# Kernel tuning notes

Hardware: AMD Instinct MI355X
Metric: run time of the kernel (lower is better)

Reference implementation:

```python
import jax, jax.numpy as jnp
import numpy as np

H = 768
NH = 12
HD = H // NH
FF = 3072
E = 4
EPS = 1e-12


def _make_expert_params(key):
    ks = jax.random.split(key, 8)
    s = 0.02
    return {
        'wq': jax.random.normal(ks[0], (H, H), jnp.float32) * s,
        'wk': jax.random.normal(ks[1], (H, H), jnp.float32) * s,
        'wv': jax.random.normal(ks[2], (H, H), jnp.float32) * s,
        'wo': jax.random.normal(ks[3], (H, H), jnp.float32) * s,
        'bq': jnp.zeros((H,), jnp.float32),
        'bk': jnp.zeros((H,), jnp.float32),
        'bv': jnp.zeros((H,), jnp.float32),
        'bo': jnp.zeros((H,), jnp.float32),
        'ln1_g': jnp.ones((H,), jnp.float32),
        'ln1_b': jnp.zeros((H,), jnp.float32),
        'w1': jax.random.normal(ks[4], (H, FF), jnp.float32) * s,
        'b1': jnp.zeros((FF,), jnp.float32),
        'w2': jax.random.normal(ks[5], (FF, H), jnp.float32) * s,
        'b2': jnp.zeros((H,), jnp.float32),
        'ln2_g': jnp.ones((H,), jnp.float32),
        'ln2_b': jnp.zeros((H,), jnp.float32),
    }


def setup_inputs() -> dict:
    key = jax.random.key(0)
    k1, k2, kp = jax.random.split(key, 3)
    hidden_states = jax.random.normal(k1, (64, 128, H), jnp.float32)
    attention_mask = jnp.zeros((64, 128), jnp.float32)  # additive mask, 0 = attend
    centers = jax.random.normal(k2, (E, H), jnp.float32)
    pkeys = jax.random.split(kp, E)
    ps = [_make_expert_params(k) for k in pkeys]
    # stack expert params along leading axis for vectorized gather-by-expert
    params = {k: jnp.stack([p[k] for p in ps], axis=0) for k in ps[0]}
    out = {'hidden_states': hidden_states, 'attention_mask': attention_mask, 'centers': centers}
    out.update(params)
    return out


def _layernorm(x, g, b):
    mu = x.mean(-1, keepdims=True)
    var = ((x - mu) ** 2).mean(-1, keepdims=True)
    return (x - mu) * jax.lax.rsqrt(var + EPS) * g + b


def _encoder(x, mask, p):
    # x: [B,S,H], mask: [B,S] additive; p: per-sample expert params (leading dim B)
    B, S, _ = x.shape
    q = jnp.einsum('bsh,bhd->bsd', x, p['wq']) + p['bq'][:, None, :]
    k = jnp.einsum('bsh,bhd->bsd', x, p['wk']) + p['bk'][:, None, :]
    v = jnp.einsum('bsh,bhd->bsd', x, p['wv']) + p['bv'][:, None, :]
    q = q.reshape(B, S, NH, HD)
    k = k.reshape(B, S, NH, HD)
    v = v.reshape(B, S, NH, HD)
    scores = jnp.einsum('bqnd,bknd->bnqk', q, k) / np.sqrt(HD).astype(np.float32)
    scores = scores + mask[:, None, None, :]
    attn = jax.nn.softmax(scores, axis=-1)
    ctx = jnp.einsum('bnqk,bknd->bqnd', attn, v).reshape(B, S, H)
    att_out = jnp.einsum('bsh,bhd->bsd', ctx, p['wo']) + p['bo'][:, None, :]
    att_out = _layernorm(att_out + x, p['ln1_g'][:, None, :], p['ln1_b'][:, None, :])
    ffn = jnp.einsum('bsh,bhf->bsf', att_out, p['w1']) + p['b1'][:, None, :]
    ffn = jax.nn.gelu(ffn)
    ffn = jnp.einsum('bsf,bfh->bsh', ffn, p['w2']) + p['b2'][:, None, :]
    out = _layernorm(att_out + ffn, p['ln2_g'][:, None, :], p['ln2_b'][:, None, :])
    return out


def reference(hidden_states, attention_mask, centers,
              wq, wk, wv, wo, bq, bk, bv, bo, ln1_g, ln1_b,
              w1, b1, w2, b2, ln2_g, ln2_b):
    # routing: mean over seq, cdist to centers, argmin -> per-sentence expert id
    h_pca = hidden_states.mean(axis=1)  # [B,H]
    d2 = (jnp.sum(h_pca ** 2, -1, keepdims=True)
          - 2.0 * h_pca @ centers.T
          + jnp.sum(centers ** 2, -1)[None, :])
    eid = jnp.argmin(d2, axis=1)  # [B]
    params = {'wq': wq, 'wk': wk, 'wv': wv, 'wo': wo, 'bq': bq, 'bk': bk,
              'bv': bv, 'bo': bo, 'ln1_g': ln1_g, 'ln1_b': ln1_b,
              'w1': w1, 'b1': b1, 'w2': w2, 'b2': b2,
              'ln2_g': ln2_g, 'ln2_b': ln2_b}
    # gather per-sample expert params (jit-friendly, honors hard routing)
    psel = {k: v[eid] for k, v in params.items()}
    return _encoder(hidden_states, attention_mask, psel)
```

## Files before the change

kernel.cpp:

```cpp
#include <hip/hip_runtime.h>
#include <hip/hip_bf16.h>
#include <math.h>

#define HDIM 768
#define NHEAD 12
#define HEADD 64
#define FFDIM 3072
#define NEXP 4
#define SEQ 128
#define NB 64
#define QKVN 2304

typedef __attribute__((ext_vector_type(8))) _Float16 f16x8;
typedef __attribute__((ext_vector_type(4))) _Float16 f16x4;
typedef __attribute__((ext_vector_type(4))) float f32x4;

__device__ __forceinline__ float gelu_fast(float x) {
  float t = -1.5957691216057308f * x * __builtin_fmaf(0.044715f * x, x, 1.0f);
  return x * __builtin_amdgcn_rcpf(1.0f + __expf(t));
}

__device__ __forceinline__ void gld_lds16(const void* g, void* l) {
  __builtin_amdgcn_global_load_lds(
      (const __attribute__((address_space(1))) unsigned int*)g,
      (__attribute__((address_space(3))) unsigned int*)l, 16, 0, 0);
}

__global__ __launch_bounds__(256) void route_cvt_kernel(
    const float* __restrict__ hs, const float* __restrict__ centers,
    int* __restrict__ eid, _Float16* __restrict__ x16) {
  int b = blockIdx.x, t = threadIdx.x;
  __shared__ float hp[HDIM];
  __shared__ float dist[NEXP];
  const float* xb = hs + (size_t)b * SEQ * HDIM;
  _Float16* ob = x16 + (size_t)b * SEQ * HDIM;

  if (t < 192) {
    float p0 = 0.f, p1 = 0.f, p2 = 0.f, p3 = 0.f;
    for (int sq = 0; sq < SEQ; ++sq) {
      float4 v = ((const float4*)(xb + (size_t)sq * HDIM))[t];
      p0 += v.x; p1 += v.y; p2 += v.z; p3 += v.w;
      f16x4 h = {(_Float16)v.x, (_Float16)v.y, (_Float16)v.z, (_Float16)v.w};
      *(f16x4*)(ob + (size_t)sq * HDIM + t * 4) = h;
    }
    hp[t * 4 + 0] = p0 * (1.0f / SEQ);
    hp[t * 4 + 1] = p1 * (1.0f / SEQ);
    hp[t * 4 + 2] = p2 * (1.0f / SEQ);
    hp[t * 4 + 3] = p3 * (1.0f / SEQ);
  }
  if (t < NEXP) dist[t] = 0.f;
  __syncthreads();

  float pe[NEXP] = {0.f, 0.f, 0.f, 0.f};
  for (int h = t; h < HDIM; h += 256) {
    float v = hp[h];
#pragma unroll
    for (int e = 0; e < NEXP; ++e) {
      float d = v - centers[e * HDIM + h];
      pe[e] += d * d;
    }
  }
#pragma unroll
  for (int e = 0; e < NEXP; ++e) atomicAdd(&dist[e], pe[e]);
  __syncthreads();
  if (t == 0) {
    int best = 0; float bv = dist[0];
    for (int e = 1; e < NEXP; ++e) if (dist[e] < bv) { bv = dist[e]; best = e; }
    eid[b] = best;
  }
}

__device__ __forceinline__ void tr_tile(const float* __restrict__ ip,
                                        _Float16* __restrict__ op,
                                        int K, int N, int nb, int kb,
                                        float (*tile)[33], int t) {
  int tx = t & 31, ty = t >> 5;
  for (int i = ty; i < 32; i += 8)
    tile[i][tx] = ip[(size_t)(kb + i) * N + nb + tx];
  __syncthreads();
  for (int i = ty; i < 32; i += 8)
    op[(size_t)(nb + i) * K + kb + tx] = (_Float16)tile[tx][i];
}

__global__ __launch_bounds__(256) void prep_weights(
    const float* __restrict__ wq, const float* __restrict__ wk,
    const float* __restrict__ wv, const float* __restrict__ wo,
    const float* __restrict__ w1, const float* __restrict__ w2,
    const float* __restrict__ bq, const float* __restrict__ bk,
    const float* __restrict__ bv,
    _Float16* __restrict__ Wqkvt, _Float16* __restrict__ Wot,
    _Float16* __restrict__ W1t, _Float16* __restrict__ W2t,
    float* __restrict__ bqkv, const int* __restrict__ eid,
    int* __restrict__ order, int* __restrict__ ord_eid) {
  __shared__ float tile[32][33];
  int x = blockIdx.x, e = blockIdx.y, t = threadIdx.x;

  if (x < 1728) {
    int which = x / 576, local = x % 576;
    const float* src = (which == 0) ? wq : (which == 1) ? wk : wv;
    tr_tile(src + (size_t)e * HDIM * HDIM,
            Wqkvt + (size_t)which * HDIM * HDIM + (size_t)e * QKVN * HDIM,
            HDIM, HDIM, (local % 24) * 32, (local / 24) * 32, tile, t);
  } else if (x < 2304) {
    int local = x - 1728;
    tr_tile(wo + (size_t)e * HDIM * HDIM, Wot + (size_t)e * HDIM * HDIM,
            HDIM, HDIM, (local % 24) * 32, (local / 24) * 32, tile, t);
  } else if (x < 4608) {
    int local = x - 2304;
    tr_tile(w1 + (size_t)e * HDIM * FFDIM, W1t + (size_t)e * FFDIM * HDIM,
            HDIM, FFDIM, (local % 96) * 32, (local / 96) * 32, tile, t);
  } else if (x < 6912) {
    int local = x - 4608;
    tr_tile(w2 + (size_t)e * FFDIM * HDIM, W2t + (size_t)e * HDIM * FFDIM,
            FFDIM, HDIM, (local % 24) * 32, (local / 24) * 32, tile, t);
  } else if (x < 6948) {
    if (e == 0) {
      int i = (x - 6912) * 256 + t;
      if (i < NEXP * QKVN) {
        int ee = i / QKVN, n = i % QKVN;
        float v = (n < HDIM) ? bq[ee * HDIM + n]
                : (n < 2 * HDIM) ? bk[ee * HDIM + n - HDIM]
                                 : bv[ee * HDIM + n - 2 * HDIM];
        bqkv[i] = v;
      }
    }
  } else {
    if (e == 0 && t == 0) {
      int n = 0;
      for (int ee = 0; ee < NEXP; ++ee)
        for (int b = 0; b < NB; ++b)
          if (eid[b] == ee) { order[n] = b; ord_eid[n] = ee; n++; }
    }
  }
}

template <int OUT_F16, int GELU, int KDIM, int SPLITK>
__global__ __launch_bounds__(256) void gemm_mfma(
    const _Float16* __restrict__ A, const _Float16* __restrict__ Wt,
    const float* __restrict__ Ball, const int* __restrict__ order,
    const int* __restrict__ ord_eid, void* __restrict__ Cv, int N) {
  constexpr int K = KDIM;
  constexpr int Kp = KDIM / SPLITK;
  constexpr int NIT = Kp / 32;
  int GX = N >> 7;
  int L = blockIdx.x;
  int low3 = L & 7, Mq = L >> 3;
  int x = Mq % GX, zhi = Mq / GX;
  int z = zhi * 8 + low3;
  int b = order[z];
  int e = ord_eid[z];
  int col0 = x * 128;
  int kz = blockIdx.y;
  int kbeg = kz * Kp;

  int t = threadIdx.x;
  int lane = t & 63, w = t >> 6;
  int quad = lane >> 4, l16 = lane & 15;
  int wr = (w >> 1) * 64, wc = (w & 1) * 64;

  __shared__ __align__(16) _Float16 As[3 * 128 * 32];
  __shared__ __align__(16) _Float16 Bs[3 * 128 * 32];

  const _Float16* Ab = A + (size_t)b * SEQ * K + kbeg;
  const _Float16* Wb = Wt + (size_t)e * N * K + (size_t)col0 * K + kbeg;

  int e0 = t * 8, e1 = 2048 + t * 8;
  int m0 = e0 >> 5, k0e = e0 & 31;
  int m1 = e1 >> 5, k1e = e1 & 31;
  const _Float16* ga0 = Ab + (size_t)m0 * K + k0e;
  const _Float16* ga1 = Ab + (size_t)m1 * K + k1e;
  const _Float16* gb0 = Wb + (size_t)m0 * K + k0e;
  const _Float16* gb1 = Wb + (size_t)m1 * K + k1e;

  auto issue = [&](int c, int st) {
    int off = c * 32;
    _Float16* Ast = As + st * 4096;
    _Float16* Bst = Bs + st * 4096;
    gld_lds16(ga0 + off, Ast + e0);
    gld_lds16(ga1 + off, Ast + e1);
    gld_lds16(gb0 + off, Bst + e0);
    gld_lds16(gb1 + off, Bst + e1);
  };

  f32x4 acc[4][4];
#pragma unroll
  for (int i = 0; i < 4; ++i)
#pragma unroll
    for (int j = 0; j < 4; ++j) acc[i][j] = (f32x4){0.f, 0.f, 0.f, 0.f};

  issue(0, 0);
  if (NIT > 1) issue(1, 1);

#pragma unroll
  for (int it = 0; it < NIT; ++it) {
    if (it < NIT - 1) __builtin_amdgcn_s_waitcnt(0xF74);
    else              __builtin_amdgcn_s_waitcnt(0xF70);
    __builtin_amdgcn_s_barrier();

    int st = it % 3;
    const _Float16* Ast = As + st * 4096;
    const _Float16* Bst = Bs + st * 4096;
    f16x8 af[4], bf[4];
#pragma unroll
    for (int i = 0; i < 4; ++i)
      af[i] = *(const f16x8*)&Ast[(wr + i * 16 + l16) * 32 + quad * 8];
#pragma unroll
    for (int i = 0; i < 4; ++i)
      bf[i] = *(const f16x8*)&Bst[(wc + i * 16 + l16) * 32 + quad * 8];
#pragma unroll
    for (int i = 0; i < 4; ++i)
#pragma unroll
      for (int j = 0; j < 4; ++j)
        acc[i][j] = __builtin_amdgcn_mfma_f32_16x16x32_f16(af[i], bf[j], acc[i][j], 0, 0, 0);

    if (it + 2 < NIT) issue(it + 2, (it + 2) % 3);
  }

  const float* bias = Ball + (size_t)e * N;

  if (OUT_F16) {
    _Float16* Ch = (_Float16*)Cv + (size_t)b * SEQ * N;
#pragma unroll
    for (int i = 0; i < 4; ++i)
#pragma unroll
      for (int j = 0; j < 4; ++j) {
        int col = col0 + wc + j * 16 + l16;
        float bv = bias[col];
#pragma unroll
        for (int r = 0; r < 4; ++r) {
          int row = wr + i * 16 + quad * 4 + r;
          float v = acc[i][j][r] + bv;
          if (GELU) v = gelu_fast(v);
          Ch[(size_t)row * N + col] = (_Float16)v;
        }
      }
  } else {
    float* Cf = (float*)Cv + (size_t)kz * NB * SEQ * N + (size_t)b * SEQ * N;
    float bscale = (kz == 0) ? 1.f : 0.f;
#pragma unroll
    for (int i = 0; i < 4; ++i)
#pragma unroll
      for (int j = 0; j < 4; ++j) {
        int col = col0 + wc + j * 16 + l16;
        float bv = bias[col] * bscale;
#pragma unroll
        for (int r = 0; r < 4; ++r) {
          int row = wr + i * 16 + quad * 4 + r;
          Cf[(size_t)row * N + col] = acc[i][j][r] + bv;
        }
      }
  }
}

__global__ __launch_bounds__(256) void attn_mfma(
    const _Float16* __restrict__ QKV, const float* __restrict__ mask,
    _Float16* __restrict__ Ctx) {
  int h = blockIdx.x, b = blockIdx.y;
  int t = threadIdx.x;
  int w = t >> 6, lane = t & 63, quad = lane >> 4, l16 = lane & 15;

  __shared__ __align__(16) char smem[54784];
  _Float16* Qs = (_Float16*)smem;
  _Float16* Ks = (_Float16*)(smem + 18432);
  _Float16* Ps = (_Float16*)smem;
  _Float16* Vt = (_Float16*)(smem + 36864);
  float* mrow = (float*)(smem + 54272);

  const _Float16* Qb = QKV + (size_t)b * SEQ * QKVN + h * HEADD;
  const _Float16* Kb = Qb + HDIM;
  const _Float16* Vb = Qb + 2 * HDIM;

#pragma unroll
  for (int it = 0; it < 4; ++it) {
    int chunk = t + it * 256;
    int row = chunk >> 3, c = chunk & 7;
    *(f16x8*)&Qs[row * 72 + c * 8] = *(const f16x8*)(Qb + (size_t)row * QKVN + c * 8);
    *(f16x8*)&Ks[row * 72 + c * 8] = *(const f16x8*)(Kb + (size_t)row * QKVN + c * 8);
  }
  {
    int vc = t & 7, vjp0 = t >> 3;
#pragma unroll
    for (int it = 0; it < 2; ++it) {
      int jp = vjp0 + it * 32;
      f16x8 v0 = *(const f16x8*)(Vb + (size_t)(2 * jp) * QKVN + vc * 8);
      f16x8 v1 = *(const f16x8*)(Vb + (size_t)(2 * jp + 1) * QKVN + vc * 8);
#pragma unroll
      for (int i = 0; i < 8; ++i) {
        int d = vc * 8 + i;
        unsigned ua = __builtin_bit_cast(unsigned short, (_Float16)v0[i]);
        unsigned ub = __builtin_bit_cast(unsigned short, (_Float16)v1[i]);
        ((unsigned*)Vt)[d * 68 + jp] = ua | (ub << 16);
      }
    }
  }
  if (t < SEQ) mrow[t] = mask[(size_t)b * SEQ + t];
  __syncthreads();

  int m0 = w * 32;
  f32x4 accs[2][8];
#pragma unroll
  for (int i = 0; i < 2; ++i)
#pragma unroll
    for (int j = 0; j < 8; ++j) accs[i][j] = (f32x4){0.f, 0.f, 0.f, 0.f};

#pragma unroll
  for (int ks = 0; ks < 2; ++ks) {
    int k0 = ks * 32 + quad * 8;
    f16x8 af[2], bf[8];
#pragma unroll
    for (int i = 0; i < 2; ++i)
      af[i] = *(const f16x8*)&Qs[(m0 + i * 16 + l16) * 72 + k0];
#pragma unroll
    for (int j = 0; j < 8; ++j)
      bf[j] = *(const f16x8*)&Ks[(j * 16 + l16) * 72 + k0];
#pragma unroll
    for (int i = 0; i < 2; ++i)
#pragma unroll
      for (int j = 0; j < 8; ++j)
        accs[i][j] = __builtin_amdgcn_mfma_f32_16x16x32_f16(af[i], bf[j], accs[i][j], 0, 0, 0);
  }
  __syncthreads();

  float mv[8];
#pragma unroll
  for (int j = 0; j < 8; ++j) mv[j] = mrow[j * 16 + l16];

  float linv[2][4];
#pragma unroll
  for (int i = 0; i < 2; ++i) {
#pragma unroll
    for (int j = 0; j < 8; ++j)
#pragma unroll
      for (int r = 0; r < 4; ++r)
        accs[i][j][r] = accs[i][j][r] * 0.125f + mv[j];
#pragma unroll
    for (int r = 0; r < 4; ++r) {
      float m = accs[i][0][r];
#pragma unroll
      for (int j = 1; j < 8; ++j) m = fmaxf(m, accs[i][j][r]);
      m = fmaxf(m, __shfl_xor(m, 1));
      m = fmaxf(m, __shfl_xor(m, 2));
      m = fmaxf(m, __shfl_xor(m, 4));
      m = fmaxf(m, __shfl_xor(m, 8));
      float sum = 0.f;
#pragma unroll
      for (int j = 0; j < 8; ++j) {
        float p = __expf(accs[i][j][r] - m);
        accs[i][j][r] = p;
        sum += p;
      }
      sum += __shfl_xor(sum, 1);
      sum += __shfl_xor(sum, 2);
      sum += __shfl_xor(sum, 4);
      sum += __shfl_xor(sum, 8);
      linv[i][r] = 1.f / sum;
    }
    int rowb = m0 + i * 16 + quad * 4;
#pragma unroll
    for (int j = 0; j < 8; ++j)
#pragma unroll
      for (int r = 0; r < 4; ++r)
        Ps[(rowb + r) * 136 + j * 16 + l16] = (_Float16)accs[i][j][r];
  }
  __syncthreads();

  f32x4 acco[2][4];
#pragma unroll
  for (int i = 0; i < 2; ++i)
#pragma unroll
    for (int j = 0; j < 4; ++j) acco[i][j] = (f32x4){0.f, 0.f, 0.f, 0.f};

#pragma unroll
  for (int ks = 0; ks < 4; ++ks) {
    int k0 = ks * 32 + quad * 8;
    f16x8 pa[2], vf[4];
#pragma unroll
    for (int i = 0; i < 2; ++i)
      pa[i] = *(const f16x8*)&Ps[(m0 + i * 16 + l16) * 136 + k0];
#pragma unroll
    for (int j = 0; j < 4; ++j)
      vf[j] = *(const f16x8*)&Vt[(j * 16 + l16) * 136 + k0];
#pragma unroll
    for (int i = 0; i < 2; ++i)
#pragma unroll
      for (int j = 0; j < 4; ++j)
        acco[i][j] = __builtin_amdgcn_mfma_f32_16x16x32_f16(pa[i], vf[j], acco[i][j], 0, 0, 0);
  }

  _Float16* Cb = Ctx + (size_t)b * SEQ * HDIM + h * HEADD;
#pragma unroll
  for (int i = 0; i < 2; ++i)
#pragma unroll
    for (int j = 0; j < 4; ++j)
#pragma unroll
      for (int r = 0; r < 4; ++r) {
        int row = m0 + i * 16 + quad * 4 + r;
        int d = j * 16 + l16;
        Cb[(size_t)row * HDIM + d] = (_Float16)(acco[i][j][r] * linv[i][r]);
      }
}

template <int NP>
__global__ __launch_bounds__(256) void resid_ln_kernel(
    const float* __restrict__ X, const float* __restrict__ P0,
    const float* __restrict__ P1,
    const float* __restrict__ Gall, const float* __restrict__ Ball,
    const int* __restrict__ eid, float* __restrict__ Out,
    _Float16* __restrict__ Out16) {
  int row = blockIdx.x, b = blockIdx.y, t = threadIdx.x;
  int e = eid[b];
  size_t off = ((size_t)b * SEQ + row) * HDIM;
  const float* x = X + off;
  const float* p0 = P0 + off;
  const float* p1 = (NP > 1) ? P1 + off : nullptr;
  float* o = Out + off;
  const float* g = Gall + (size_t)e * HDIM;
  const float* bb = Ball + (size_t)e * HDIM;

  __shared__ float buf[HDIM];
  __shared__ float red[256];

  float s = 0.f;
  for (int h = t; h < HDIM; h += 256) {
    float v = x[h] + p0[h];
    if (NP > 1) v += p1[h];
    buf[h] = v;
    s += v;
  }
  red[t] = s;
  __syncthreads();
  for (int off2 = 128; off2 > 0; off2 >>= 1) {
    if (t < off2) red[t] += red[t + off2];
    __syncthreads();
  }
  float mean = red[0] * (1.0f / HDIM);
  __syncthreads();

  float s2 = 0.f;
  for (int h = t; h < HDIM; h += 256) {
    float d = buf[h] - mean;
    s2 += d * d;
  }
  red[t] = s2;
  __syncthreads();
  for (int off2 = 128; off2 > 0; off2 >>= 1) {
    if (t < off2) red[t] += red[t + off2];
    __syncthreads();
  }
  float var = red[0] * (1.0f / HDIM);
  float rs = rsqrtf(var + 1e-12f);

  for (int h = t; h < HDIM; h += 256) {
    float v = (buf[h] - mean) * rs * g[h] + bb[h];
    o[h] = v;
    if (Out16) Out16[off + h] = (_Float16)v;
  }
}

extern "C" void kernel_launch(void* const* d_in, const int* in_sizes, int n_in,
                              void* d_out, int out_size, void* d_ws, size_t ws_size,
                              hipStream_t stream) {
  const float* hs   = (const float*)d_in[0];
  const float* mask = (const float*)d_in[1];
  const float* cen  = (const float*)d_in[2];
  const float* wq = (const float*)d_in[3];
  const float* wk = (const float*)d_in[4];
  const float* wv = (const float*)d_in[5];
  const float* wo = (const float*)d_in[6];
  const float* bq = (const float*)d_in[7];
  const float* bk = (const float*)d_in[8];
  const float* bv = (const float*)d_in[9];
  const float* bo = (const float*)d_in[10];
  const float* ln1g = (const float*)d_in[11];
  const float* ln1b = (const float*)d_in[12];
  const float* w1 = (const float*)d_in[13];
  const float* b1 = (const float*)d_in[14];
  const float* w2 = (const float*)d_in[15];
  const float* b2 = (const float*)d_in[16];
  const float* ln2g = (const float*)d_in[17];
  const float* ln2b = (const float*)d_in[18];
  float* out = (float*)d_out;

  const size_t sh = (size_t)SEQ * HDIM;

  char* p = (char*)d_ws;
  int* eid = (int*)p;                 p += 256;
  int* order = (int*)p;               p += 256;
  int* ord_eid = (int*)p;             p += 256;
  float* bqkv = (float*)p;            p += (size_t)NEXP * QKVN * 4;
  _Float16* Wqkvt = (_Float16*)p;     p += (size_t)NEXP * QKVN * HDIM * 2;
  _Float16* Wot = (_Float16*)p;       p += (size_t)NEXP * HDIM * HDIM * 2;
  _Float16* W1t = (_Float16*)p;       p += (size_t)NEXP * FFDIM * HDIM * 2;
  _Float16* W2t = (_Float16*)p;       p += (size_t)NEXP * HDIM * FFDIM * 2;
  _Float16* x16 = (_Float16*)p;       p += (size_t)NB * sh * 2;

  char* region = p;                   p += (size_t)NB * SEQ * QKVN * 2;
  _Float16* ctx16 = (_Float16*)p;     p += (size_t)NB * sh * 2;
  float* aof = (float*)p;             p += (size_t)NB * sh * 4;
  _Float16* ao16 = (_Float16*)p;      p += (size_t)NB * sh * 2;
  char* ffreg = p;                    p += (size_t)NB * SEQ * FFDIM * 2;

  float* woparts = (float*)ffreg;
  float* w2parts = (float*)region;
  _Float16* ff16 = (_Float16*)ffreg;

  route_cvt_kernel<<<NB, 256, 0, stream>>>(hs, cen, eid, x16);
  prep_weights<<<dim3(6949, NEXP), 256, 0, stream>>>(
      wq, wk, wv, wo, w1, w2, bq, bk, bv,
      Wqkvt, Wot, W1t, W2t, bqkv, eid, order, ord_eid);
  gemm_mfma<1, 0, HDIM, 1><<<dim3((QKVN / 128) * NB, 1), 256, 0, stream>>>(
      x16, Wqkvt, bqkv, order, ord_eid, region, QKVN);
  attn_mfma<<<dim3(NHEAD, NB), 256, 0, stream>>>(
      (const _Float16*)region, mask, ctx16);
  gemm_mfma<0, 0, HDIM, 2><<<dim3((HDIM / 128) * NB, 2), 256, 0, stream>>>(
      ctx16, Wot, bo, order, ord_eid, woparts, HDIM);
  resid_ln_kernel<2><<<dim3(SEQ, NB), 256, 0, stream>>>(
      hs, woparts, woparts + (size_t)NB * sh, ln1g, ln1b, eid, aof, ao16);
  gemm_mfma<1, 1, HDIM, 1><<<dim3((FFDIM / 128) * NB, 1), 256, 0, stream>>>(
      ao16, W1t, b1, order, ord_eid, ff16, FFDIM);
  gemm_mfma<0, 0, FFDIM, 2><<<dim3((HDIM / 128) * NB, 2), 256, 0, stream>>>(
      ff16, W2t, b2, order, ord_eid, w2parts, HDIM);
  resid_ln_kernel<2><<<dim3(SEQ, NB), 256, 0, stream>>>(
      aof, w2parts, w2parts + (size_t)NB * sh, ln2g, ln2b, eid, out,
      (_Float16*)nullptr);
}
```

Before: 461.9 us.

## Widen GEMM tiles to 128x256 with XOR-swizzled LDS and double buffering

The expert GEMM tile grows from 128x128 to 128x256. Each wave now covers all 128 rows and a 64-column strip, so A fragments are reused across more columns and fewer blocks are launched. The LDS layout gets an XOR swizzle on the k-offset to reduce bank conflicts, and the pipeline drops from triple to double buffering with a full wait each iteration. Launch bounds ask for 2 blocks per CU. Risks: higher accumulator register pressure (128 floats per thread), less load/compute overlap, and fewer blocks for the split-K N=768 GEMMs.

```diff
diff --git a/kernel.cpp b/kernel.cpp
--- a/kernel.cpp
+++ b/kernel.cpp
@@ -135,85 +135,84 @@
 }
 
 template <int OUT_F16, int GELU, int KDIM, int SPLITK>
-__global__ __launch_bounds__(256) void gemm_mfma(
+__global__ __launch_bounds__(256, 2) void gemm_mfma(
     const _Float16* __restrict__ A, const _Float16* __restrict__ Wt,
     const float* __restrict__ Ball, const int* __restrict__ order,
     const int* __restrict__ ord_eid, void* __restrict__ Cv, int N) {
   constexpr int K = KDIM;
   constexpr int Kp = KDIM / SPLITK;
   constexpr int NIT = Kp / 32;
-  int GX = N >> 7;
+  int GX = N >> 8;
   int L = blockIdx.x;
   int low3 = L & 7, Mq = L >> 3;
   int x = Mq % GX, zhi = Mq / GX;
   int z = zhi * 8 + low3;
   int b = order[z];
   int e = ord_eid[z];
-  int col0 = x * 128;
+  int col0 = x * 256;
   int kz = blockIdx.y;
   int kbeg = kz * Kp;
 
   int t = threadIdx.x;
   int lane = t & 63, w = t >> 6;
   int quad = lane >> 4, l16 = lane & 15;
-  int wr = (w >> 1) * 64, wc = (w & 1) * 64;
-
-  __shared__ __align__(16) _Float16 As[3 * 128 * 32];
-  __shared__ __align__(16) _Float16 Bs[3 * 128 * 32];
+  int wc = w * 64;
+
+  __shared__ __align__(16) _Float16 As[2 * 128 * 32];
+  __shared__ __align__(16) _Float16 Bs[2 * 256 * 32];
+
+  int ksw = ((t & 3) ^ ((t >> 2) & 3) ^ ((t >> 4) & 3)) * 8;
+  int r0 = t >> 2;
 
   const _Float16* Ab = A + (size_t)b * SEQ * K + kbeg;
   const _Float16* Wb = Wt + (size_t)e * N * K + (size_t)col0 * K + kbeg;
-
-  int e0 = t * 8, e1 = 2048 + t * 8;
-  int m0 = e0 >> 5, k0e = e0 & 31;
-  int m1 = e1 >> 5, k1e = e1 & 31;
-  const _Float16* ga0 = Ab + (size_t)m0 * K + k0e;
-  const _Float16* ga1 = Ab + (size_t)m1 * K + k1e;
-  const _Float16* gb0 = Wb + (size_t)m0 * K + k0e;
-  const _Float16* gb1 = Wb + (size_t)m1 * K + k1e;
+  const _Float16* ga0 = Ab + (size_t)r0 * K + ksw;
+  const _Float16* gb0 = Wb + (size_t)r0 * K + ksw;
 
   auto issue = [&](int c, int st) {
     int off = c * 32;
     _Float16* Ast = As + st * 4096;
-    _Float16* Bst = Bs + st * 4096;
-    gld_lds16(ga0 + off, Ast + e0);
-    gld_lds16(ga1 + off, Ast + e1);
-    gld_lds16(gb0 + off, Bst + e0);
-    gld_lds16(gb1 + off, Bst + e1);
+    _Float16* Bst = Bs + st * 8192;
+    gld_lds16(ga0 + off, Ast + t * 8);
+    gld_lds16(ga0 + 64 * K + off, Ast + 2048 + t * 8);
+    gld_lds16(gb0 + off, Bst + t * 8);
+    gld_lds16(gb0 + 64 * K + off, Bst + 2048 + t * 8);
+    gld_lds16(gb0 + 128 * K + off, Bst + 4096 + t * 8);
+    gld_lds16(gb0 + 192 * K + off, Bst + 6144 + t * 8);
   };
 
-  f32x4 acc[4][4];
-#pragma unroll
-  for (int i = 0; i < 4; ++i)
+  f32x4 acc[8][4];
+#pragma unroll
+  for (int i = 0; i < 8; ++i)
 #pragma unroll
     for (int j = 0; j < 4; ++j) acc[i][j] = (f32x4){0.f, 0.f, 0.f, 0.f};
 
+  int sl = (l16 & 3) ^ ((l16 >> 2) & 3);
+  int kread = (quad ^ sl) * 8;
+
   issue(0, 0);
-  if (NIT > 1) issue(1, 1);
-
-#pragma unroll
+
+#pragma unroll 2
   for (int it = 0; it < NIT; ++it) {
-    if (it < NIT - 1) __builtin_amdgcn_s_waitcnt(0xF74);
-    else              __builtin_amdgcn_s_waitcnt(0xF70);
+    __builtin_amdgcn_s_waitcnt(0xF70);
     __builtin_amdgcn_s_barrier();
-
-    int st = it % 3;
+    if (it + 1 < NIT) issue(it + 1, (it + 1) & 1);
+
+    int st = it & 1;
     const _Float16* Ast = As + st * 4096;
-    const _Float16* Bst = Bs + st * 4096;
-    f16x8 af[4], bf[4];
-#pragma unroll
-    for (int i = 0; i < 4; ++i)
-      af[i] = *(const f16x8*)&Ast[(wr + i * 16 + l16) * 32 + quad * 8];
-#pragma unroll
-    for (int i = 0; i < 4; ++i)
-      bf[i] = *(const f16x8*)&Bst[(wc + i * 16 + l16) * 32 + quad * 8];
-#pragma unroll
-    for (int i = 0; i < 4; ++i)
+    const _Float16* Bst = Bs + st * 8192;
+    f16x8 af[8], bf[4];
+#pragma unroll
+    for (int i = 0; i < 8; ++i)
+      af[i] = *(const f16x8*)&Ast[(i * 16 + l16) * 32 + kread];
+#pragma unroll
+    for (int j = 0; j < 4; ++j)
+      bf[j] = *(const f16x8*)&Bst[(wc + j * 16 + l16) * 32 + kread];
+#pragma unroll
+    for (int i = 0; i < 8; ++i)
 #pragma unroll
       for (int j = 0; j < 4; ++j)
         acc[i][j] = __builtin_amdgcn_mfma_f32_16x16x32_f16(af[i], bf[j], acc[i][j], 0, 0, 0);
-
-    if (it + 2 < NIT) issue(it + 2, (it + 2) % 3);
   }
 
   const float* bias = Ball + (size_t)e * N;
@@ -221,14 +220,14 @@
   if (OUT_F16) {
     _Float16* Ch = (_Float16*)Cv + (size_t)b * SEQ * N;
 #pragma unroll
-    for (int i = 0; i < 4; ++i)
+    for (int i = 0; i < 8; ++i)
 #pragma unroll
       for (int j = 0; j < 4; ++j) {
         int col = col0 + wc + j * 16 + l16;
         float bv = bias[col];
 #pragma unroll
         for (int r = 0; r < 4; ++r) {
-          int row = wr + i * 16 + quad * 4 + r;
+          int row = i * 16 + quad * 4 + r;
           float v = acc[i][j][r] + bv;
           if (GELU) v = gelu_fast(v);
           Ch[(size_t)row * N + col] = (_Float16)v;
@@ -238,14 +237,14 @@
     float* Cf = (float*)Cv + (size_t)kz * NB * SEQ * N + (size_t)b * SEQ * N;
     float bscale = (kz == 0) ? 1.f : 0.f;
 #pragma unroll
-    for (int i = 0; i < 4; ++i)
+    for (int i = 0; i < 8; ++i)
 #pragma unroll
       for (int j = 0; j < 4; ++j) {
         int col = col0 + wc + j * 16 + l16;
         float bv = bias[col] * bscale;
 #pragma unroll
         for (int r = 0; r < 4; ++r) {
-          int row = wr + i * 16 + quad * 4 + r;
+          int row = i * 16 + quad * 4 + r;
           Cf[(size_t)row * N + col] = acc[i][j][r] + bv;
         }
       }
@@ -508,17 +507,17 @@
   prep_weights<<<dim3(6949, NEXP), 256, 0, stream>>>(
       wq, wk, wv, wo, w1, w2, bq, bk, bv,
       Wqkvt, Wot, W1t, W2t, bqkv, eid, order, ord_eid);
-  gemm_mfma<1, 0, HDIM, 1><<<dim3((QKVN / 128) * NB, 1), 256, 0, stream>>>(
+  gemm_mfma<1, 0, HDIM, 1><<<dim3((QKVN / 256) * NB, 1), 256, 0, stream>>>(
       x16, Wqkvt, bqkv, order, ord_eid, region, QKVN);
   attn_mfma<<<dim3(NHEAD, NB), 256, 0, stream>>>(
       (const _Float16*)region, mask, ctx16);
-  gemm_mfma<0, 0, HDIM, 2><<<dim3((HDIM / 128) * NB, 2), 256, 0, stream>>>(
+  gemm_mfma<0, 0, HDIM, 2><<<dim3((HDIM / 256) * NB, 2), 256, 0, stream>>>(
       ctx16, Wot, bo, order, ord_eid, woparts, HDIM);
   resid_ln_kernel<2><<<dim3(SEQ, NB), 256, 0, stream>>>(
       hs, woparts, woparts + (size_t)NB * sh, ln1g, ln1b, eid, aof, ao16);
-  gemm_mfma<1, 1, HDIM, 1><<<dim3((FFDIM / 128) * NB, 1), 256, 0, stream>>>(
+  gemm_mfma<1, 1, HDIM, 1><<<dim3((FFDIM / 256) * NB, 1), 256, 0, stream>>>(
       ao16, W1t, b1, order, ord_eid, ff16, FFDIM);
-  gemm_mfma<0, 0, FFDIM, 2><<<dim3((HDIM / 128) * NB, 2), 256, 0, stream>>>(
+  gemm_mfma<0, 0, FFDIM, 2><<<dim3((HDIM / 256) * NB, 2), 256, 0, stream>>>(
       ff16, W2t, b2, order, ord_eid, w2parts, HDIM);
   resid_ln_kernel<2><<<dim3(SEQ, NB), 256, 0, stream>>>(
       aof, w2parts, w2parts + (size_t)NB * sh, ln2g, ln2b, eid, out,
```

New measurement: 484.6 us. +4.9%, slower.

## Rewrite expert GEMM as 8-wave 128x256 tile with swizzled double-buffered LDS

Applied to the files above, without the earlier changes.

Replaces the 4-wave 128x128 GEMM with an 8-wave (512-thread) kernel computing 128x256 tiles with K-steps of 64 split into two halves. It double-buffers through 96KB of dynamic LDS using direct global-to-LDS loads, XOR-swizzles LDS columns to avoid bank conflicts, and raises wave priority around the MFMA blocks. Blocks are remapped in an XCD-aware order so blocks sharing an expert's weights land together. The larger tile halves A reloads per output. In exchange it launches fewer workgroups and uses more LDS per block, which may limit occupancy.

```diff
diff --git a/kernel.cpp b/kernel.cpp
--- a/kernel.cpp
+++ b/kernel.cpp
@@ -14,6 +14,10 @@
 typedef __attribute__((ext_vector_type(8))) _Float16 f16x8;
 typedef __attribute__((ext_vector_type(4))) _Float16 f16x4;
 typedef __attribute__((ext_vector_type(4))) float f32x4;
+
+#define WAITVM3 __builtin_amdgcn_s_waitcnt(0xF73)
+#define WAITVM0 __builtin_amdgcn_s_waitcnt(0xF70)
+#define WAITLGKM0 __builtin_amdgcn_s_waitcnt(0xC07F)
 
 __device__ __forceinline__ float gelu_fast(float x) {
   float t = -1.5957691216057308f * x * __builtin_fmaf(0.044715f * x, x, 1.0f);
@@ -135,51 +139,48 @@
 }
 
 template <int OUT_F16, int GELU, int KDIM, int SPLITK>
-__global__ __launch_bounds__(256) void gemm_mfma(
+__global__ __launch_bounds__(512, 2) void gemm_mfma8(
     const _Float16* __restrict__ A, const _Float16* __restrict__ Wt,
     const float* __restrict__ Ball, const int* __restrict__ order,
     const int* __restrict__ ord_eid, void* __restrict__ Cv, int N) {
   constexpr int K = KDIM;
   constexpr int Kp = KDIM / SPLITK;
-  constexpr int NIT = Kp / 32;
-  int GX = N >> 7;
+  constexpr int NT = Kp / 64;
+  extern __shared__ __align__(16) char dynlds[];
+  _Float16* lds = (_Float16*)dynlds;
+
+  int GX = N >> 8;
+  int nwg = GX * NB * SPLITK;
   int L = blockIdx.x;
-  int low3 = L & 7, Mq = L >> 3;
-  int x = Mq % GX, zhi = Mq / GX;
-  int z = zhi * 8 + low3;
+  int r = (L & 7) * (nwg >> 3) + (L >> 3);
+  int z = r & 63;
+  int rest = r >> 6;
+  int kz = rest % SPLITK;
+  int c = rest / SPLITK;
   int b = order[z];
   int e = ord_eid[z];
-  int col0 = x * 128;
-  int kz = blockIdx.y;
+  int col0 = c * 256;
   int kbeg = kz * Kp;
 
   int t = threadIdx.x;
   int lane = t & 63, w = t >> 6;
   int quad = lane >> 4, l16 = lane & 15;
-  int wr = (w >> 1) * 64, wc = (w & 1) * 64;
-
-  __shared__ __align__(16) _Float16 As[3 * 128 * 32];
-  __shared__ __align__(16) _Float16 Bs[3 * 128 * 32];
-
-  const _Float16* Ab = A + (size_t)b * SEQ * K + kbeg;
-  const _Float16* Wb = Wt + (size_t)e * N * K + (size_t)col0 * K + kbeg;
-
-  int e0 = t * 8, e1 = 2048 + t * 8;
-  int m0 = e0 >> 5, k0e = e0 & 31;
-  int m1 = e1 >> 5, k1e = e1 & 31;
-  const _Float16* ga0 = Ab + (size_t)m0 * K + k0e;
-  const _Float16* ga1 = Ab + (size_t)m1 * K + k1e;
-  const _Float16* gb0 = Wb + (size_t)m0 * K + k0e;
-  const _Float16* gb1 = Wb + (size_t)m1 * K + k1e;
-
-  auto issue = [&](int c, int st) {
-    int off = c * 32;
-    _Float16* Ast = As + st * 4096;
-    _Float16* Bst = Bs + st * 4096;
-    gld_lds16(ga0 + off, Ast + e0);
-    gld_lds16(ga1 + off, Ast + e1);
-    gld_lds16(gb0 + off, Bst + e0);
-    gld_lds16(gb1 + off, Bst + e1);
+  int wr64 = (w >> 2) * 64;
+  int wc64 = (w & 3) * 64;
+
+  int csw = ((t & 3) ^ ((t >> 2) & 3) ^ ((t >> 4) & 3)) * 8;
+  int r0 = t >> 2;
+
+  const _Float16* srcA = A + (size_t)b * SEQ * K + kbeg + (size_t)r0 * K + csw;
+  const _Float16* srcB0 = Wt + (size_t)e * N * K + (size_t)(col0 + r0) * K + kbeg + csw;
+  const _Float16* srcB1 = srcB0 + (size_t)128 * K;
+
+  auto issueH = [&](int Tn, int h) {
+    _Float16* dst = lds + (size_t)(Tn & 1) * 24576;
+    int goff = Tn * 64 + h * 32;
+    gld_lds16(srcA + goff, dst + h * 4096 + t * 8);
+    gld_lds16(srcB0 + goff, dst + 8192 + h * 8192 + t * 8);
+    gld_lds16(srcB1 + goff, dst + 8192 + h * 8192 + 4096 + t * 8);
   };
 
   f32x4 acc[4][4];
@@ -188,32 +189,68 @@
 #pragma unroll
     for (int j = 0; j < 4; ++j) acc[i][j] = (f32x4){0.f, 0.f, 0.f, 0.f};
 
-  issue(0, 0);
-  if (NIT > 1) issue(1, 1);
-
-#pragma unroll
-  for (int it = 0; it < NIT; ++it) {
-    if (it < NIT - 1) __builtin_amdgcn_s_waitcnt(0xF74);
-    else              __builtin_amdgcn_s_waitcnt(0xF70);
-    __builtin_amdgcn_s_barrier();
-
-    int st = it % 3;
-    const _Float16* Ast = As + st * 4096;
-    const _Float16* Bst = Bs + st * 4096;
-    f16x8 af[4], bf[4];
-#pragma unroll
-    for (int i = 0; i < 4; ++i)
-      af[i] = *(const f16x8*)&Ast[(wr + i * 16 + l16) * 32 + quad * 8];
-#pragma unroll
-    for (int i = 0; i < 4; ++i)
-      bf[i] = *(const f16x8*)&Bst[(wc + i * 16 + l16) * 32 + quad * 8];
-#pragma unroll
-    for (int i = 0; i < 4; ++i)
+  int sl = (l16 & 3) ^ ((l16 >> 2) & 3);
+  int ck8 = (quad ^ sl) * 8;
+
+  issueH(0, 0);
+  issueH(0, 1);
+  WAITVM3;
+  __builtin_amdgcn_s_barrier();
+
+#pragma unroll 2
+  for (int T = 0; T < NT; ++T) {
+    int bi = T & 1;
+    const _Float16* Ab = lds + (size_t)bi * 24576;
+    const _Float16* Bb = Ab + 8192;
+
+    {
+      f16x8 af[4], bf[4];
+#pragma unroll
+      for (int i = 0; i < 4; ++i)
+        af[i] = *(const f16x8*)&Ab[(wr64 + i * 16 + l16) * 32 + ck8];
 #pragma unroll
       for (int j = 0; j < 4; ++j)
-        acc[i][j] = __builtin_amdgcn_mfma_f32_16x16x32_f16(af[i], bf[j], acc[i][j], 0, 0, 0);
-
-    if (it + 2 < NIT) issue(it + 2, (it + 2) % 3);
+        bf[j] = *(const f16x8*)&Bb[(wc64 + j * 16 + l16) * 32 + ck8];
+      if (T + 1 < NT) issueH(T + 1, 0);
+      __builtin_amdgcn_s_barrier();
+      WAITLGKM0;
+      __builtin_amdgcn_s_setprio(1);
+#pragma unroll
+      for (int i = 0; i < 4; ++i)
+#pragma unroll
+        for (int j = 0; j < 4; ++j)
+          acc[i][j] = __builtin_amdgcn_mfma_f32_16x16x32_f16(af[i], bf[j], acc[i][j], 0, 0, 0);
+      __builtin_amdgcn_s_setprio(0);
+      if (T + 1 < NT) WAITVM3;
+      else            WAITVM0;
+      __builtin_amdgcn_s_barrier();
+    }
+
+    {
+      const _Float16* Ab1 = Ab + 4096;
+      const _Float16* Bb1 = Bb + 8192;
+      f16x8 af[4], bf[4];
+#pragma unroll
+      for (int i = 0; i < 4; ++i)
+        af[i] = *(const f16x8*)&Ab1[(wr64 + i * 16 + l16) * 32 + ck8];
+#pragma unroll
+      for (int j = 0; j < 4; ++j)
+        bf[j] = *(const f16x8*)&Bb1[(wc64 + j * 16 + l16) * 32 + ck8];
+      if (T + 1 < NT) issueH(T + 1, 1);
+      __builtin_amdgcn_s_barrier();
+      WAITLGKM0;
+      __builtin_amdgcn_s_setprio(1);
+#pragma unroll
+      for (int i = 0; i < 4; ++i)
+#pragma unroll
+        for (int j = 0; j < 4; ++j)
+          acc[i][j] = __builtin_amdgcn_mfma_f32_16x16x32_f16(af[i], bf[j], acc[i][j], 0, 0, 0);
+      __builtin_amdgcn_s_setprio(0);
+      if (T + 1 < NT) {
+        WAITVM3;
+        __builtin_amdgcn_s_barrier();
+      }
+    }
   }
 
   const float* bias = Ball + (size_t)e * N;
@@ -224,12 +261,12 @@
     for (int i = 0; i < 4; ++i)
 #pragma unroll
       for (int j = 0; j < 4; ++j) {
-        int col = col0 + wc + j * 16 + l16;
+        int col = col0 + wc64 + j * 16 + l16;
         float bv = bias[col];
 #pragma unroll
-        for (int r = 0; r < 4; ++r) {
-          int row = wr + i * 16 + quad * 4 + r;
-          float v = acc[i][j][r] + bv;
+        for (int r2 = 0; r2 < 4; ++r2) {
+          int row = wr64 + i * 16 + quad * 4 + r2;
+          float v = acc[i][j][r2] + bv;
           if (GELU) v = gelu_fast(v);
           Ch[(size_t)row * N + col] = (_Float16)v;
         }
@@ -241,12 +278,12 @@
     for (int i = 0; i < 4; ++i)
 #pragma unroll
       for (int j = 0; j < 4; ++j) {
-        int col = col0 + wc + j * 16 + l16;
+        int col = col0 + wc64 + j * 16 + l16;
         float bv = bias[col] * bscale;
 #pragma unroll
-        for (int r = 0; r < 4; ++r) {
-          int row = wr + i * 16 + quad * 4 + r;
-          Cf[(size_t)row * N + col] = acc[i][j][r] + bv;
+        for (int r2 = 0; r2 < 4; ++r2) {
+          int row = wr64 + i * 16 + quad * 4 + r2;
+          Cf[(size_t)row * N + col] = acc[i][j][r2] + bv;
         }
       }
   }
@@ -482,6 +519,20 @@
   float* out = (float*)d_out;
 
   const size_t sh = (size_t)SEQ * HDIM;
+  const int DYNLDS = 98304;
+
+  static bool attr_done = false;
+  if (!attr_done) {
+    attr_done = true;
+    auto* k1 = gemm_mfma8<1, 0, HDIM, 1>;
+    auto* k2 = gemm_mfma8<0, 0, HDIM, 2>;
+    auto* k3 = gemm_mfma8<1, 1, HDIM, 1>;
+    auto* k4 = gemm_mfma8<0, 0, FFDIM, 2>;
+    (void)hipFuncSetAttribute((const void*)k1, hipFuncAttributeMaxDynamicSharedMemorySize, DYNLDS);
+    (void)hipFuncSetAttribute((const void*)k2, hipFuncAttributeMaxDynamicSharedMemorySize, DYNLDS);
+    (void)hipFuncSetAttribute((const void*)k3, hipFuncAttributeMaxDynamicSharedMemorySize, DYNLDS);
+    (void)hipFuncSetAttribute((const void*)k4, hipFuncAttributeMaxDynamicSharedMemorySize, DYNLDS);
+  }
 
   char* p = (char*)d_ws;
   int* eid = (int*)p;                 p += 256;
@@ -508,17 +559,17 @@
   prep_weights<<<dim3(6949, NEXP), 256, 0, stream>>>(
       wq, wk, wv, wo, w1, w2, bq, bk, bv,
       Wqkvt, Wot, W1t, W2t, bqkv, eid, order, ord_eid);
-  gemm_mfma<1, 0, HDIM, 1><<<dim3((QKVN / 128) * NB, 1), 256, 0, stream>>>(
+  gemm_mfma8<1, 0, HDIM, 1><<<dim3((QKVN / 256) * NB), 512, DYNLDS, stream>>>(
       x16, Wqkvt, bqkv, order, ord_eid, region, QKVN);
   attn_mfma<<<dim3(NHEAD, NB), 256, 0, stream>>>(
       (const _Float16*)region, mask, ctx16);
-  gemm_mfma<0, 0, HDIM, 2><<<dim3((HDIM / 128) * NB, 2), 256, 0, stream>>>(
+  gemm_mfma8<0, 0, HDIM, 2><<<dim3((HDIM / 256) * NB * 2), 512, DYNLDS, stream>>>(
       ctx16, Wot, bo, order, ord_eid, woparts, HDIM);
   resid_ln_kernel<2><<<dim3(SEQ, NB), 256, 0, stream>>>(
       hs, woparts, woparts + (size_t)NB * sh, ln1g, ln1b, eid, aof, ao16);
-  gemm_mfma<1, 1, HDIM, 1><<<dim3((FFDIM / 128) * NB, 1), 256, 0, stream>>>(
+  gemm_mfma8<1, 1, HDIM, 1><<<dim3((FFDIM / 256) * NB), 512, DYNLDS, stream>>>(
       ao16, W1t, b1, order, ord_eid, ff16, FFDIM);
-  gemm_mfma<0, 0, FFDIM, 2><<<dim3((HDIM / 128) * NB, 2), 256, 0, stream>>>(
+  gemm_mfma8<0, 0, FFDIM, 2><<<dim3((HDIM / 256) * NB * 2), 512, DYNLDS, stream>>>(
       ff16, W2t, b2, order, ord_eid, w2parts, HDIM);
   resid_ln_kernel<2><<<dim3(SEQ, NB), 256, 0, stream>>>(
       aof, w2parts, w2parts + (size_t)NB * sh, ln2g, ln2b, eid, out,
```

Measured after the change: 488.8 us. 1.06x slower.
